# Performance work log

Measured on AMD Instinct MI355X. Metric: run time of the kernel, lower is better.

The kernel has to match this reference:

```python
import jax, jax.numpy as jnp
import numpy as np

B, C, L = 1024, 256, 16   # nodes, channels (num_features), num_ell (dim of 0e+1o+2e+3o)
E = 10                    # num_elements
K3, K2, K1 = 23, 4, 1     # U-matrix path counts for correlation orders 3,2,1


def setup_inputs() -> dict:
    key = jax.random.key(0)
    ks = jax.random.split(key, 8)
    return {
        "x": jax.random.normal(ks[0], (B, C, L), jnp.float32),
        "y": jax.random.normal(ks[1], (B, E), jnp.float32),
        # U buffers (generalized Clebsch-Gordan, here random stand-ins of the right shapes)
        "U3": jax.random.normal(ks[2], (L, L, L, K3), jnp.float32),
        "U2": jax.random.normal(ks[3], (L, L, K2), jnp.float32),
        "U1": jax.random.normal(ks[4], (L, K1), jnp.float32),
        # per-element weights, scaled by 1/num_params as in the module
        "W3": jax.random.normal(ks[5], (E, K3, C), jnp.float32) / K3,
        "W2": jax.random.normal(ks[6], (E, K2, C), jnp.float32) / K2,
        "W1": jax.random.normal(ks[7], (E, K1, C), jnp.float32) / K1,
    }


def reference(x, y, U3, U2, U1, W3, W2, W1):
    # symmetric_cp, irrep_out lmax=0 (scalar output), correlation=3.
    # Main (nu=3): out[b,c,w,v] = sum_{i,k,e} U3[w,v,i,k] W3[e,k,c] x[b,c,i] y[b,e]
    # Efficient order: element-select weights, outer-product over (i,k), then one GEMM with U3.
    w3 = jnp.einsum('ekc,be->bkc', W3, y)              # [B,K3,C]
    q = jnp.einsum('bkc,bci->bcik', w3, x)             # [B,C,L,K3]
    out = jnp.einsum('wvik,bcik->bcwv', U3, q)         # [B,C,L,L]
    # nu=2: weighting then feature contraction
    w2 = jnp.einsum('ekc,be->bkc', W2, y)              # [B,K2,C]
    c2 = jnp.einsum('wvk,bkc->bcwv', U2, w2) + out     # [B,C,L,L]
    out = jnp.einsum('bcwi,bci->bcw', c2, x)           # [B,C,L]
    # nu=1
    w1 = jnp.einsum('ekc,be->bkc', W1, y)              # [B,K1,C]
    c1 = jnp.einsum('wk,bkc->bcw', U1, w1) + out       # [B,C,L]
    out = jnp.einsum('bci,bci->bc', c1, x)             # [B,C]
    return out.reshape(out.shape[0], -1)
```

## Files before the change

kernel.cpp:

```cpp
#include <hip/hip_runtime.h>


#define B_   1024
#define C_   256
#define L_   16
#define E_   10
#define K3_  23
#define K2_  4

#define NM3  816
#define NM2  136
#define MTOT 992
#define NCH  31
#define SPSTR 20
#define STSTR 260

using f32x4   = __attribute__((ext_vector_type(4))) float;
using short8v = __attribute__((ext_vector_type(8))) short;

__device__ __host__ __forceinline__ constexpr int tri_(int n) { return n * (n + 1) / 2; }
__device__ __host__ __forceinline__ constexpr int tet_(int n) { return n * (n + 1) * (n + 2) / 6; }

struct MTab { unsigned char a[MTOT], b[MTOT], c[MTOT]; };
constexpr MTab mkMT() {
  MTab t = {};
  int m = 0;
  for (int a = 0; a < 16; a++)
    for (int b = a; b < 16; b++)
      for (int c = b; c < 16; c++) { t.a[m] = a; t.b[m] = b; t.c[m] = c; ++m; }
  for (int a = 0; a < 16; a++)
    for (int b = a; b < 16; b++) { t.a[m] = a; t.b[m] = b; t.c[m] = 16; ++m; }
  for (int a = 0; a < 16; a++) { t.a[m] = a; t.b[m] = 16; t.c[m] = 16; ++m; }
  while (m < MTOT) { t.a[m] = 17; t.b[m] = 17; t.c[m] = 17; ++m; }
  return t;
}
constexpr MTab MT = mkMT();

__global__ void prep_kernel(const float* __restrict__ U3, const float* __restrict__ U2,
                            const float* __restrict__ U1, unsigned short* __restrict__ wsFrag) {
  __shared__ float sRow[32][33];
  const int ch = blockIdx.x;
  const int tid = threadIdx.x;
  if (tid < 32) {
    const int m = ch * 32 + tid;
    for (int i = 0; i < 32; i++) sRow[tid][i] = 0.f;
    if (m < NM3) {
      int ia = 0;
      while (tet_(16) - tet_(16 - (ia + 1)) <= m) ia++;
      int rem = m - (tet_(16) - tet_(16 - ia));
      int ib = ia;
      while (tri_(16 - ia) - tri_(16 - (ib + 1)) <= rem) ib++;
      int ic = ib + (rem - (tri_(16 - ia) - tri_(16 - ib)));
      int pw[6] = {ia, ia, ib, ib, ic, ic};
      int pv[6] = {ib, ic, ia, ic, ia, ib};
      int pi[6] = {ic, ib, ic, ia, ib, ia};
      bool use[6];
      for (int p = 0; p < 6; p++) {
        bool dup = false;
        for (int q = 0; q < p; q++)
          dup = dup || (pw[p] == pw[q] && pv[p] == pv[q] && pi[p] == pi[q]);
        use[p] = !dup;
      }
      for (int k = 0; k < K3_; k++) {
        float s = 0.f;
        for (int p = 0; p < 6; p++)
          if (use[p]) s += U3[((pw[p] * L_ + pv[p]) * L_ + pi[p]) * K3_ + k];
        sRow[tid][k] = s;
      }
    } else if (m < NM3 + NM2) {
      const int pidx = m - NM3;
      int ia = 0;
      while (136 - tri_(16 - (ia + 1)) <= pidx) ia++;
      int ib = ia + (pidx - (136 - tri_(16 - ia)));
      for (int k2 = 0; k2 < K2_; k2++) {
        float s = U2[(ia * L_ + ib) * K2_ + k2];
        if (ia != ib) s += U2[(ib * L_ + ia) * K2_ + k2];
        sRow[tid][23 + k2] = s;
      }
    } else if (m < NM3 + NM2 + L_) {
      sRow[tid][27] = U1[m - NM3 - NM2];
    }
  }
  __syncthreads();
  if (tid < 128) {
    const int lane = tid & 63, kt = (tid >> 6) & 1;
    unsigned short hi[8], lo[8];
    for (int j = 0; j < 8; j++) {
      float v = sRow[(lane >> 4) * 8 + j][kt * 16 + (lane & 15)];
      unsigned vb = __float_as_uint(v);
      unsigned short h = (unsigned short)(vb >> 16);
      float l = v - __uint_as_float(((unsigned)h) << 16);
      hi[j] = h;
      lo[j] = (unsigned short)(__float_as_uint(l) >> 16);
    }
    unsigned* dst0 = (unsigned*)(wsFrag + ((size_t)((ch * 2 + kt) * 2 + 0) * 64 + lane) * 8);
    unsigned* dst1 = (unsigned*)(wsFrag + ((size_t)((ch * 2 + kt) * 2 + 1) * 64 + lane) * 8);
    for (int p = 0; p < 4; p++) {
      dst0[p] = (unsigned)hi[2 * p] | ((unsigned)hi[2 * p + 1] << 16);
      dst1[p] = (unsigned)lo[2 * p] | ((unsigned)lo[2 * p + 1] << 16);
    }
  }
}

#define BIDX(ch, kt, part) ((((ch) * 2 + (kt)) * 2 + (part)) * 64 + lane)

template <int CH>
__device__ __forceinline__ void chunk_body(
    const float (&XX)[18], unsigned* pr, const unsigned* aptr,
    const float4* __restrict__ Bg, int lane, float4 (&nb)[4], f32x4 (&acc)[4][2]) {
  #pragma unroll
  for (int g = 0; g < 4; ++g) {
    unsigned pk[4];
    #pragma unroll
    for (int q = 0; q < 4; ++q) {
      const int m0 = CH * 32 + 2 * (g * 4 + q);
      float p0 = XX[MT.a[m0]] * XX[MT.b[m0]] * XX[MT.c[m0]];
      float p1 = XX[MT.a[m0 + 1]] * XX[MT.b[m0 + 1]] * XX[MT.c[m0 + 1]];
      asm("v_cvt_pk_bf16_f32 %0, %1, %2" : "=v"(pk[q]) : "v"(p0), "v"(p1));
    }
    *(uint4*)(pr + 4 * g) = make_uint4(pk[0], pk[1], pk[2], pk[3]);
  }

  float4 b00 = nb[0], b01 = nb[1], b10 = nb[2], b11 = nb[3];
  if constexpr (CH + 1 < NCH) {
    nb[0] = Bg[BIDX(CH + 1, 0, 0)];
    nb[1] = Bg[BIDX(CH + 1, 0, 1)];
    nb[2] = Bg[BIDX(CH + 1, 1, 0)];
    nb[3] = Bg[BIDX(CH + 1, 1, 1)];
  }
  short8v B00, B01, B10, B11;
  __builtin_memcpy(&B00, &b00, 16); __builtin_memcpy(&B01, &b01, 16);
  __builtin_memcpy(&B10, &b10, 16); __builtin_memcpy(&B11, &b11, 16);

  #pragma unroll
  for (int rt = 0; rt < 4; ++rt) {
    short8v A;
    __builtin_memcpy(&A, aptr + rt * 16 * SPSTR, 16);
    acc[rt][0] = __builtin_amdgcn_mfma_f32_16x16x32_bf16(A, B00, acc[rt][0], 0, 0, 0);
    acc[rt][0] = __builtin_amdgcn_mfma_f32_16x16x32_bf16(A, B01, acc[rt][0], 0, 0, 0);
    acc[rt][1] = __builtin_amdgcn_mfma_f32_16x16x32_bf16(A, B10, acc[rt][1], 0, 0, 0);
    acc[rt][1] = __builtin_amdgcn_mfma_f32_16x16x32_bf16(A, B11, acc[rt][1], 0, 0, 0);
  }
}

template <int CH>
struct Loop {
  static __device__ __forceinline__ void run(
      const float (&XX)[18], unsigned* pr, const unsigned* aptr,
      const float4* __restrict__ Bg, int lane, float4 (&nb)[4], f32x4 (&acc)[4][2]) {
    chunk_body<CH>(XX, pr, aptr, Bg, lane, nb, acc);
    Loop<CH + 1>::run(XX, pr, aptr, Bg, lane, nb, acc);
  }
};
template <>
struct Loop<NCH> {
  static __device__ __forceinline__ void run(
      const float (&)[18], unsigned*, const unsigned*,
      const float4* __restrict__, int, float4 (&)[4], f32x4 (&)[4][2]) {}
};

__global__ __launch_bounds__(256, 3) void symcon_kernel(
    const float* __restrict__ x,
    const float* __restrict__ y,
    const float* __restrict__ W3,
    const float* __restrict__ W2,
    const float* __restrict__ W1,
    const unsigned short* __restrict__ wsFrag,
    float* __restrict__ out)
{
  __shared__ float smem[28 * STSTR];
  unsigned* sP = (unsigned*)smem;
  float* sT = smem;

  const int tid = threadIdx.x, c = tid, b = blockIdx.x;
  const int lane = tid & 63;

  float XX[18];
  {
    const float4* xg = (const float4*)(x + ((size_t)b * C_ + c) * L_);
    #pragma unroll
    for (int i = 0; i < 4; i++) {
      float4 v = xg[i];
      XX[i * 4 + 0] = v.x; XX[i * 4 + 1] = v.y;
      XX[i * 4 + 2] = v.z; XX[i * 4 + 3] = v.w;
    }
    XX[16] = 1.f; XX[17] = 0.f;
  }

  const float4* Bg = (const float4*)wsFrag;
  float4 nb[4];
  nb[0] = Bg[BIDX(0, 0, 0)]; nb[1] = Bg[BIDX(0, 0, 1)];
  nb[2] = Bg[BIDX(0, 1, 0)]; nb[3] = Bg[BIDX(0, 1, 1)];

  f32x4 acc[4][2];
  #pragma unroll
  for (int rt = 0; rt < 4; rt++)
    #pragma unroll
    for (int kt = 0; kt < 2; kt++) acc[rt][kt] = (f32x4)0.f;

  unsigned* pr = sP + tid * SPSTR;
  const unsigned* aptr = sP + ((tid & 192) + (tid & 15)) * SPSTR + ((tid >> 4) & 3) * 4;

  Loop<0>::run(XX, pr, aptr, Bg, lane, nb, acc);

  __syncthreads();
  const int wrow = tid & 192;
  #pragma unroll
  for (int rt = 0; rt < 4; ++rt) {
    const int c0 = wrow + rt * 16 + ((tid >> 4) & 3) * 4;
    {
      const int k = tid & 15;
      *(f32x4*)&sT[k * STSTR + c0] = acc[rt][0];
    }
    if ((tid & 15) < 12) {
      const int k = 16 + (tid & 15);
      *(f32x4*)&sT[k * STSTR + c0] = acc[rt][1];
    }
  }
  float t[28];
  #pragma unroll
  for (int k = 0; k < 28; ++k) t[k] = sT[k * STSTR + tid];

  float yreg[E_];
  #pragma unroll
  for (int e = 0; e < E_; e++) yreg[e] = y[b * E_ + e];

  float result = 0.f;
  #pragma unroll
  for (int k = 0; k < K3_; k++) {
    const float* w3p = &W3[k * C_ + c];
    float w3k = 0.f;
    #pragma unroll
    for (int e = 0; e < E_; e++) w3k += w3p[e * K3_ * C_] * yreg[e];
    result += t[k] * w3k;
  }
  #pragma unroll
  for (int k2 = 0; k2 < K2_; k2++) {
    const float* w2p = &W2[k2 * C_ + c];
    float w2k = 0.f;
    #pragma unroll
    for (int e = 0; e < E_; e++) w2k += w2p[e * K2_ * C_] * yreg[e];
    result += t[23 + k2] * w2k;
  }
  {
    float w1v = 0.f;
    #pragma unroll
    for (int e = 0; e < E_; e++) w1v += W1[e * C_ + c] * yreg[e];
    result += t[27] * w1v;
  }

  out[(size_t)b * C_ + c] = result;
}

extern "C" void kernel_launch(void* const* d_in, const int* in_sizes, int n_in,
                              void* d_out, int out_size, void* d_ws, size_t ws_size,
                              hipStream_t stream) {
  const float* x  = (const float*)d_in[0];
  const float* y  = (const float*)d_in[1];
  const float* U3 = (const float*)d_in[2];
  const float* U2 = (const float*)d_in[3];
  const float* U1 = (const float*)d_in[4];
  const float* W3 = (const float*)d_in[5];
  const float* W2 = (const float*)d_in[6];
  const float* W1 = (const float*)d_in[7];
  float* out = (float*)d_out;

  unsigned short* wsFrag = (unsigned short*)d_ws;

  prep_kernel<<<dim3(NCH), dim3(256), 0, stream>>>(U3, U2, U1, wsFrag);
  symcon_kernel<<<dim3(B_), dim3(256), 0, stream>>>(
      x, y, W3, W2, W1, wsFrag, out);
}
```

Measured before the change: 136.7 us.

## Double-buffer LDS product tiles and interleave independent MFMA chains

```diff
diff --git a/kernel.cpp b/kernel.cpp
--- a/kernel.cpp
+++ b/kernel.cpp
@@ -13,6 +13,7 @@
 #define MTOT 992
 #define NCH  31
 #define SPSTR 20
+#define SPBUF (256 * SPSTR)
 #define STSTR 260
 
 using f32x4   = __attribute__((ext_vector_type(4))) float;
@@ -105,9 +106,8 @@
 #define BIDX(ch, kt, part) ((((ch) * 2 + (kt)) * 2 + (part)) * 64 + lane)
 
 template <int CH>
-__device__ __forceinline__ void chunk_body(
-    const float (&XX)[18], unsigned* pr, const unsigned* aptr,
-    const float4* __restrict__ Bg, int lane, float4 (&nb)[4], f32x4 (&acc)[4][2]) {
+__device__ __forceinline__ void p_store(const float (&XX)[18], unsigned* sP, int tid) {
+  unsigned* pr = sP + (CH & 1) * SPBUF + tid * SPSTR;
   #pragma unroll
   for (int g = 0; g < 4; ++g) {
     unsigned pk[4];
@@ -120,6 +120,18 @@
     }
     *(uint4*)(pr + 4 * g) = make_uint4(pk[0], pk[1], pk[2], pk[3]);
   }
+}
+
+template <int CH>
+__device__ __forceinline__ void chunk_body(
+    const float (&XX)[18], unsigned* sP, const unsigned* aptrBase,
+    const float4* __restrict__ Bg, int lane, int tid,
+    float4 (&nb)[4], f32x4 (&acc)[4][2]) {
+  const unsigned* ap = aptrBase + (CH & 1) * SPBUF;
+  short8v A[4];
+  #pragma unroll
+  for (int rt = 0; rt < 4; ++rt)
+    __builtin_memcpy(&A[rt], ap + rt * 16 * SPSTR, 16);
 
   float4 b00 = nb[0], b01 = nb[1], b10 = nb[2], b11 = nb[3];
   if constexpr (CH + 1 < NCH) {
@@ -127,39 +139,44 @@
     nb[1] = Bg[BIDX(CH + 1, 0, 1)];
     nb[2] = Bg[BIDX(CH + 1, 1, 0)];
     nb[3] = Bg[BIDX(CH + 1, 1, 1)];
+    p_store<CH + 1>(XX, sP, tid);
   }
   short8v B00, B01, B10, B11;
   __builtin_memcpy(&B00, &b00, 16); __builtin_memcpy(&B01, &b01, 16);
   __builtin_memcpy(&B10, &b10, 16); __builtin_memcpy(&B11, &b11, 16);
 
   #pragma unroll
-  for (int rt = 0; rt < 4; ++rt) {
-    short8v A;
-    __builtin_memcpy(&A, aptr + rt * 16 * SPSTR, 16);
-    acc[rt][0] = __builtin_amdgcn_mfma_f32_16x16x32_bf16(A, B00, acc[rt][0], 0, 0, 0);
-    acc[rt][0] = __builtin_amdgcn_mfma_f32_16x16x32_bf16(A, B01, acc[rt][0], 0, 0, 0);
-    acc[rt][1] = __builtin_amdgcn_mfma_f32_16x16x32_bf16(A, B10, acc[rt][1], 0, 0, 0);
-    acc[rt][1] = __builtin_amdgcn_mfma_f32_16x16x32_bf16(A, B11, acc[rt][1], 0, 0, 0);
-  }
+  for (int rt = 0; rt < 4; ++rt)
+    acc[rt][0] = __builtin_amdgcn_mfma_f32_16x16x32_bf16(A[rt], B00, acc[rt][0], 0, 0, 0);
+  #pragma unroll
+  for (int rt = 0; rt < 4; ++rt)
+    acc[rt][1] = __builtin_amdgcn_mfma_f32_16x16x32_bf16(A[rt], B10, acc[rt][1], 0, 0, 0);
+  #pragma unroll
+  for (int rt = 0; rt < 4; ++rt)
+    acc[rt][0] = __builtin_amdgcn_mfma_f32_16x16x32_bf16(A[rt], B01, acc[rt][0], 0, 0, 0);
+  #pragma unroll
+  for (int rt = 0; rt < 4; ++rt)
+    acc[rt][1] = __builtin_amdgcn_mfma_f32_16x16x32_bf16(A[rt], B11, acc[rt][1], 0, 0, 0);
 }
 
 template <int CH>
 struct Loop {
   static __device__ __forceinline__ void run(
-      const float (&XX)[18], unsigned* pr, const unsigned* aptr,
-      const float4* __restrict__ Bg, int lane, float4 (&nb)[4], f32x4 (&acc)[4][2]) {
-    chunk_body<CH>(XX, pr, aptr, Bg, lane, nb, acc);
-    Loop<CH + 1>::run(XX, pr, aptr, Bg, lane, nb, acc);
+      const float (&XX)[18], unsigned* sP, const unsigned* aptrBase,
+      const float4* __restrict__ Bg, int lane, int tid,
+      float4 (&nb)[4], f32x4 (&acc)[4][2]) {
+    chunk_body<CH>(XX, sP, aptrBase, Bg, lane, tid, nb, acc);
+    Loop<CH + 1>::run(XX, sP, aptrBase, Bg, lane, tid, nb, acc);
   }
 };
 template <>
 struct Loop<NCH> {
   static __device__ __forceinline__ void run(
       const float (&)[18], unsigned*, const unsigned*,
-      const float4* __restrict__, int, float4 (&)[4], f32x4 (&)[4][2]) {}
+      const float4* __restrict__, int, int, float4 (&)[4], f32x4 (&)[4][2]) {}
 };
 
-__global__ __launch_bounds__(256, 3) void symcon_kernel(
+__global__ __launch_bounds__(256, 4) void symcon_kernel(
     const float* __restrict__ x,
     const float* __restrict__ y,
     const float* __restrict__ W3,
@@ -168,9 +185,9 @@
     const unsigned short* __restrict__ wsFrag,
     float* __restrict__ out)
 {
-  __shared__ float smem[28 * STSTR];
-  unsigned* sP = (unsigned*)smem;
-  float* sT = smem;
+  __shared__ unsigned smemU[2 * SPBUF];
+  unsigned* sP = smemU;
+  float* sT = (float*)smemU;
 
   const int tid = threadIdx.x, c = tid, b = blockIdx.x;
   const int lane = tid & 63;
@@ -198,10 +215,11 @@
     #pragma unroll
     for (int kt = 0; kt < 2; kt++) acc[rt][kt] = (f32x4)0.f;
 
-  unsigned* pr = sP + tid * SPSTR;
-  const unsigned* aptr = sP + ((tid & 192) + (tid & 15)) * SPSTR + ((tid >> 4) & 3) * 4;
-
-  Loop<0>::run(XX, pr, aptr, Bg, lane, nb, acc);
+  const unsigned* aptrBase =
+      sP + ((tid & 192) + (tid & 15)) * SPSTR + ((tid >> 4) & 3) * 4;
+
+  p_store<0>(XX, sP, tid);
+  Loop<0>::run(XX, sP, aptrBase, Bg, lane, tid, nb, acc);
 
   __syncthreads();
   const int wrow = tid & 192;
```

Result: slower. 151.1 us (+10.5%).
